# Optimization experiments

Hardware: AMD Instinct MI355X
Metric: run time of the kernel (lower is better)

## Reference

```python
import jax, jax.numpy as jnp
import numpy as np

B = 64        # graphs per batch
N_ATOMS = 16384   # atoms per graph
N_GLOBAL = 8      # global (virtual) nodes per graph
EPS = 1e-8


def setup_inputs() -> dict:
    key = jax.random.key(0)
    k1, k2, k3 = jax.random.split(key, 3)
    N = B * N_ATOMS
    G = B * N_GLOBAL
    atom_positions = jax.random.normal(k1, (N, 3), dtype=jnp.float32)
    pred_pos_global_node = jax.random.normal(k2, (G, 3), dtype=jnp.float32)
    true_direction_vectors = jax.random.normal(k3, (N, 3), dtype=jnp.float32)
    # uniform sorted batch assignment (equal-sized graphs)
    atom_batch_index = jnp.repeat(jnp.arange(B, dtype=jnp.int64), N_ATOMS)
    global_node_batch_index = jnp.repeat(jnp.arange(B, dtype=jnp.int64), N_GLOBAL)
    return {
        "atom_positions": atom_positions,
        "pred_pos_global_node": pred_pos_global_node,
        "true_direction_vectors": true_direction_vectors,
        "atom_batch_index": atom_batch_index,
        "global_node_batch_index": global_node_batch_index,
        "num_graphs": B,
    }


def reference(atom_positions, pred_pos_global_node, true_direction_vectors,
              atom_batch_index, global_node_batch_index, num_graphs):
    # Uniform batching: reshape ragged segments into dense [B, n] / [B, G].
    N = atom_positions.shape[0]
    Gt = pred_pos_global_node.shape[0]
    n = N // num_graphs
    G = Gt // num_graphs
    atoms = atom_positions.reshape(num_graphs, 1, n, 3)          # [B,1,n,3]
    tdir = true_direction_vectors.reshape(num_graphs, 1, n, 3)   # [B,1,n,3]
    gpos = pred_pos_global_node.reshape(num_graphs, G, 1, 3)     # [B,G,1,3]
    pdir = gpos - atoms                                           # [B,G,n,3] pred direction vectors
    num = jnp.sum(tdir * pdir, axis=-1)                           # [B,G,n]
    den = jnp.maximum(
        jnp.linalg.norm(tdir, axis=-1) * jnp.linalg.norm(pdir, axis=-1), EPS)
    cos = num / den                                               # [B,G,n]
    cosine_losses = 1.0 - jnp.mean(cos, axis=-1)                  # [B,G]
    min_idx = jnp.argmin(cosine_losses, axis=-1)                  # [B]
    min_loss = jnp.min(cosine_losses, axis=-1)                    # [B]
    return jnp.mean(min_loss), min_idx
```

## Files before the change

### kernel.cpp

```cpp
#include <hip/hip_runtime.h>

constexpr int B_GRAPHS = 64;
constexpr int N_PER_GRAPH = 16384;
constexpr int GPN = 8;
constexpr int THREADS = 256;
constexpr int ATOMS_PER_THREAD = 4;
constexpr int BLOCKS_PER_GRAPH = N_PER_GRAPH / (THREADS * ATOMS_PER_THREAD);
constexpr int NBLOCKS = B_GRAPHS * BLOCKS_PER_GRAPH;

__global__ __launch_bounds__(THREADS) void cos_partial(
    const float* __restrict__ atom_pos,
    const float* __restrict__ gpos,
    const float* __restrict__ tdir,
    float* __restrict__ partials)
{
    const int b  = blockIdx.x / BLOCKS_PER_GRAPH;
    const int tg = blockIdx.x * THREADS + threadIdx.x;

    const float4* ap4 = (const float4*)atom_pos;
    const float4* td4 = (const float4*)tdir;
    const size_t fb = (size_t)tg * 3;
    const float4 a0 = ap4[fb + 0], a1 = ap4[fb + 1], a2 = ap4[fb + 2];
    const float4 t0 = td4[fb + 0], t1 = td4[fb + 1], t2 = td4[fb + 2];

    float gx[GPN], gy[GPN], gz[GPN];
    const float* gp = gpos + (size_t)b * GPN * 3;
#pragma unroll
    for (int g = 0; g < GPN; ++g) {
        gx[g] = gp[g * 3 + 0];
        gy[g] = gp[g * 3 + 1];
        gz[g] = gp[g * 3 + 2];
    }

    const float ax[4] = {a0.x, a0.w, a1.z, a2.y};
    const float ay[4] = {a0.y, a1.x, a1.w, a2.z};
    const float az[4] = {a0.z, a1.y, a2.x, a2.w};
    const float tx[4] = {t0.x, t0.w, t1.z, t2.y};
    const float ty[4] = {t0.y, t1.x, t1.w, t2.z};
    const float tz[4] = {t0.z, t1.y, t2.x, t2.w};

    float accg[GPN];
#pragma unroll
    for (int g = 0; g < GPN; ++g) accg[g] = 0.0f;

#pragma unroll
    for (int a = 0; a < 4; ++a) {
        const float tn2 = fmaf(tx[a], tx[a], fmaf(ty[a], ty[a], tz[a] * tz[a]));
        const float itn = __builtin_amdgcn_rsqf(fmaxf(tn2, 1e-20f));
#pragma unroll
        for (int g = 0; g < GPN; ++g) {
            const float dx = gx[g] - ax[a];
            const float dy = gy[g] - ay[a];
            const float dz = gz[g] - az[a];
            const float dot = fmaf(tx[a], dx, fmaf(ty[a], dy, tz[a] * dz));
            const float pn2 = fmaf(dx, dx, fmaf(dy, dy, dz * dz));
            const float ipn = __builtin_amdgcn_rsqf(fmaxf(pn2, 1e-20f));
            accg[g] = fmaf(dot * itn, ipn, accg[g]);
        }
    }

    const int lane = threadIdx.x & 63;
    const int wave = threadIdx.x >> 6;
#pragma unroll
    for (int g = 0; g < GPN; ++g) {
        float v = accg[g];
#pragma unroll
        for (int off = 32; off > 0; off >>= 1)
            v += __shfl_xor(v, off);
        accg[g] = v;
    }

    __shared__ float lsum[THREADS / 64][GPN];
    if (lane == 0) {
#pragma unroll
        for (int g = 0; g < GPN; ++g) lsum[wave][g] = accg[g];
    }
    __syncthreads();
    if (threadIdx.x < GPN) {
        const int g = threadIdx.x;
        float s = 0.0f;
#pragma unroll
        for (int w = 0; w < THREADS / 64; ++w) s += lsum[w][g];
        partials[(size_t)blockIdx.x * GPN + g] = s;
    }
}

__global__ __launch_bounds__(512) void finalize(
    const float* __restrict__ partials,
    float* __restrict__ out)
{
    __shared__ float sums[B_GRAPHS * GPN];
    const int t = threadIdx.x;
    const int b = t >> 3, g = t & 7;
    float s = 0.0f;
#pragma unroll
    for (int c = 0; c < BLOCKS_PER_GRAPH; ++c)
        s += partials[((size_t)(b * BLOCKS_PER_GRAPH + c)) * GPN + g];
    sums[t] = s;
    __syncthreads();

    if (t < B_GRAPHS) {
        float minloss = 1e30f;
        int minidx = 0;
#pragma unroll
        for (int g2 = 0; g2 < GPN; ++g2) {
            const float loss = 1.0f - sums[t * GPN + g2] * (1.0f / (float)N_PER_GRAPH);
            if (loss < minloss) {
                minloss = loss;
                minidx = g2;
            }
        }
        out[1 + t] = (float)minidx;
        float v = minloss;
#pragma unroll
        for (int off = 32; off > 0; off >>= 1)
            v += __shfl_down(v, off);
        if (t == 0) out[0] = v * (1.0f / (float)B_GRAPHS);
    }
}

extern "C" void kernel_launch(void* const* d_in, const int* in_sizes, int n_in,
                              void* d_out, int out_size, void* d_ws, size_t ws_size,
                              hipStream_t stream) {
    const float* atom_pos = (const float*)d_in[0];
    const float* gpos     = (const float*)d_in[1];
    const float* tdir     = (const float*)d_in[2];

    float* partials = (float*)d_ws;

    cos_partial<<<NBLOCKS, THREADS, 0, stream>>>(atom_pos, gpos, tdir, partials);
    finalize<<<1, 512, 0, stream>>>(partials, (float*)d_out);
}
```

Before: 85.31 us.

## Fuse finalize into main kernel via last-block ticket and halve atoms per thread

New measurement: 150.6 us. 1.77x slower.

```diff
diff --git a/kernel.cpp b/kernel.cpp
--- a/kernel.cpp
+++ b/kernel.cpp
@@ -4,24 +4,27 @@
 constexpr int N_PER_GRAPH = 16384;
 constexpr int GPN = 8;
 constexpr int THREADS = 256;
-constexpr int ATOMS_PER_THREAD = 4;
+constexpr int ATOMS_PER_THREAD = 2;
 constexpr int BLOCKS_PER_GRAPH = N_PER_GRAPH / (THREADS * ATOMS_PER_THREAD);
 constexpr int NBLOCKS = B_GRAPHS * BLOCKS_PER_GRAPH;
+constexpr size_t PARTIALS_FLOATS = (size_t)NBLOCKS * GPN;
 
-__global__ __launch_bounds__(THREADS) void cos_partial(
+__global__ __launch_bounds__(THREADS) void cos_fused(
     const float* __restrict__ atom_pos,
     const float* __restrict__ gpos,
     const float* __restrict__ tdir,
-    float* __restrict__ partials)
+    float* __restrict__ partials,
+    unsigned int* __restrict__ ticket,
+    float* __restrict__ out)
 {
     const int b  = blockIdx.x / BLOCKS_PER_GRAPH;
     const int tg = blockIdx.x * THREADS + threadIdx.x;
 
-    const float4* ap4 = (const float4*)atom_pos;
-    const float4* td4 = (const float4*)tdir;
+    const float2* ap2 = (const float2*)atom_pos;
+    const float2* td2 = (const float2*)tdir;
     const size_t fb = (size_t)tg * 3;
-    const float4 a0 = ap4[fb + 0], a1 = ap4[fb + 1], a2 = ap4[fb + 2];
-    const float4 t0 = td4[fb + 0], t1 = td4[fb + 1], t2 = td4[fb + 2];
+    const float2 a0 = ap2[fb + 0], a1 = ap2[fb + 1], a2 = ap2[fb + 2];
+    const float2 t0 = td2[fb + 0], t1 = td2[fb + 1], t2 = td2[fb + 2];
 
     float gx[GPN], gy[GPN], gz[GPN];
     const float* gp = gpos + (size_t)b * GPN * 3;
@@ -32,19 +35,19 @@
         gz[g] = gp[g * 3 + 2];
     }
 
-    const float ax[4] = {a0.x, a0.w, a1.z, a2.y};
-    const float ay[4] = {a0.y, a1.x, a1.w, a2.z};
-    const float az[4] = {a0.z, a1.y, a2.x, a2.w};
-    const float tx[4] = {t0.x, t0.w, t1.z, t2.y};
-    const float ty[4] = {t0.y, t1.x, t1.w, t2.z};
-    const float tz[4] = {t0.z, t1.y, t2.x, t2.w};
+    const float ax[2] = {a0.x, a1.y};
+    const float ay[2] = {a0.y, a2.x};
+    const float az[2] = {a1.x, a2.y};
+    const float tx[2] = {t0.x, t1.y};
+    const float ty[2] = {t0.y, t2.x};
+    const float tz[2] = {t1.x, t2.y};
 
     float accg[GPN];
 #pragma unroll
     for (int g = 0; g < GPN; ++g) accg[g] = 0.0f;
 
 #pragma unroll
-    for (int a = 0; a < 4; ++a) {
+    for (int a = 0; a < 2; ++a) {
         const float tn2 = fmaf(tx[a], tx[a], fmaf(ty[a], ty[a], tz[a] * tz[a]));
         const float itn = __builtin_amdgcn_rsqf(fmaxf(tn2, 1e-20f));
 #pragma unroll
@@ -59,63 +62,78 @@
         }
     }
 
-    const int lane = threadIdx.x & 63;
-    const int wave = threadIdx.x >> 6;
 #pragma unroll
     for (int g = 0; g < GPN; ++g) {
         float v = accg[g];
-#pragma unroll
-        for (int off = 32; off > 0; off >>= 1)
-            v += __shfl_xor(v, off);
+        v += __shfl_xor(v, 8);
+        v += __shfl_xor(v, 16);
+        v += __shfl_xor(v, 32);
         accg[g] = v;
     }
+    const int lane = threadIdx.x & 63;
+    const int wave = threadIdx.x >> 6;
+    const int myg = lane >> 3;
+    float s = accg[0];
+#pragma unroll
+    for (int g = 1; g < GPN; ++g) s = (myg == g) ? accg[g] : s;
+    s += __shfl_xor(s, 1);
+    s += __shfl_xor(s, 2);
+    s += __shfl_xor(s, 4);
 
     __shared__ float lsum[THREADS / 64][GPN];
-    if (lane == 0) {
-#pragma unroll
-        for (int g = 0; g < GPN; ++g) lsum[wave][g] = accg[g];
+    __shared__ float sums[B_GRAPHS * GPN];
+    __shared__ unsigned int s_isLast;
+    if ((lane & 7) == 0) lsum[wave][myg] = s;
+    __syncthreads();
+
+    if (threadIdx.x < GPN) {
+        const int g = threadIdx.x;
+        const float bs = lsum[0][g] + lsum[1][g] + lsum[2][g] + lsum[3][g];
+        __hip_atomic_store(&partials[(size_t)blockIdx.x * GPN + g], bs,
+                           __ATOMIC_RELAXED, __HIP_MEMORY_SCOPE_AGENT);
     }
     __syncthreads();
-    if (threadIdx.x < GPN) {
-        const int g = threadIdx.x;
-        float s = 0.0f;
+
+    if (threadIdx.x == 0) {
+        __threadfence();
+        const unsigned int old = __hip_atomic_fetch_add(
+            ticket, 1u, __ATOMIC_ACQ_REL, __HIP_MEMORY_SCOPE_AGENT);
+        s_isLast = (old == (unsigned int)(NBLOCKS - 1)) ? 1u : 0u;
+    }
+    __syncthreads();
+    if (s_isLast == 0u) return;
+
+    __threadfence();
+    for (int p = threadIdx.x; p < B_GRAPHS * GPN; p += THREADS) {
+        const int bb = p >> 3, g = p & 7;
+        float s2 = 0.0f;
 #pragma unroll
-        for (int w = 0; w < THREADS / 64; ++w) s += lsum[w][g];
-        partials[(size_t)blockIdx.x * GPN + g] = s;
+        for (int c = 0; c < BLOCKS_PER_GRAPH; ++c)
+            s2 += __hip_atomic_load(
+                &partials[(size_t)(bb * BLOCKS_PER_GRAPH + c) * GPN + g],
+                __ATOMIC_RELAXED, __HIP_MEMORY_SCOPE_AGENT);
+        sums[p] = s2;
     }
-}
-
-__global__ __launch_bounds__(512) void finalize(
-    const float* __restrict__ partials,
-    float* __restrict__ out)
-{
-    __shared__ float sums[B_GRAPHS * GPN];
-    const int t = threadIdx.x;
-    const int b = t >> 3, g = t & 7;
-    float s = 0.0f;
-#pragma unroll
-    for (int c = 0; c < BLOCKS_PER_GRAPH; ++c)
-        s += partials[((size_t)(b * BLOCKS_PER_GRAPH + c)) * GPN + g];
-    sums[t] = s;
     __syncthreads();
 
-    if (t < B_GRAPHS) {
+    if (threadIdx.x < B_GRAPHS) {
+        const int bb = threadIdx.x;
         float minloss = 1e30f;
         int minidx = 0;
 #pragma unroll
-        for (int g2 = 0; g2 < GPN; ++g2) {
-            const float loss = 1.0f - sums[t * GPN + g2] * (1.0f / (float)N_PER_GRAPH);
+        for (int g = 0; g < GPN; ++g) {
+            const float loss = 1.0f - sums[bb * GPN + g] * (1.0f / (float)N_PER_GRAPH);
             if (loss < minloss) {
                 minloss = loss;
-                minidx = g2;
+                minidx = g;
             }
         }
-        out[1 + t] = (float)minidx;
+        out[1 + bb] = (float)minidx;
         float v = minloss;
 #pragma unroll
         for (int off = 32; off > 0; off >>= 1)
             v += __shfl_down(v, off);
-        if (t == 0) out[0] = v * (1.0f / (float)B_GRAPHS);
+        if (bb == 0) out[0] = v * (1.0f / (float)B_GRAPHS);
     }
 }
 
@@ -126,8 +144,10 @@
     const float* gpos     = (const float*)d_in[1];
     const float* tdir     = (const float*)d_in[2];
 
-    float* partials = (float*)d_ws;
+    float* partials      = (float*)d_ws;
+    unsigned int* ticket = (unsigned int*)((char*)d_ws + PARTIALS_FLOATS * sizeof(float));
 
-    cos_partial<<<NBLOCKS, THREADS, 0, stream>>>(atom_pos, gpos, tdir, partials);
-    finalize<<<1, 512, 0, stream>>>(partials, (float*)d_out);
+    hipMemsetAsync(ticket, 0, sizeof(unsigned int), stream);
+    cos_fused<<<NBLOCKS, THREADS, 0, stream>>>(
+        atom_pos, gpos, tdir, partials, ticket, (float*)d_out);
 }
```

## Halve atoms per thread and use transposed butterfly wave reduction

Applied to the files above, without the earlier changes.

Result: no change. 83.87 us (-1.7%).

```diff
diff --git a/kernel.cpp b/kernel.cpp
--- a/kernel.cpp
+++ b/kernel.cpp
@@ -4,7 +4,7 @@
 constexpr int N_PER_GRAPH = 16384;
 constexpr int GPN = 8;
 constexpr int THREADS = 256;
-constexpr int ATOMS_PER_THREAD = 4;
+constexpr int ATOMS_PER_THREAD = 2;
 constexpr int BLOCKS_PER_GRAPH = N_PER_GRAPH / (THREADS * ATOMS_PER_THREAD);
 constexpr int NBLOCKS = B_GRAPHS * BLOCKS_PER_GRAPH;
 
@@ -17,11 +17,11 @@
     const int b  = blockIdx.x / BLOCKS_PER_GRAPH;
     const int tg = blockIdx.x * THREADS + threadIdx.x;
 
-    const float4* ap4 = (const float4*)atom_pos;
-    const float4* td4 = (const float4*)tdir;
+    const float2* ap2 = (const float2*)atom_pos;
+    const float2* td2 = (const float2*)tdir;
     const size_t fb = (size_t)tg * 3;
-    const float4 a0 = ap4[fb + 0], a1 = ap4[fb + 1], a2 = ap4[fb + 2];
-    const float4 t0 = td4[fb + 0], t1 = td4[fb + 1], t2 = td4[fb + 2];
+    const float2 a0 = ap2[fb + 0], a1 = ap2[fb + 1], a2 = ap2[fb + 2];
+    const float2 t0 = td2[fb + 0], t1 = td2[fb + 1], t2 = td2[fb + 2];
 
     float gx[GPN], gy[GPN], gz[GPN];
     const float* gp = gpos + (size_t)b * GPN * 3;
@@ -32,19 +32,19 @@
         gz[g] = gp[g * 3 + 2];
     }
 
-    const float ax[4] = {a0.x, a0.w, a1.z, a2.y};
-    const float ay[4] = {a0.y, a1.x, a1.w, a2.z};
-    const float az[4] = {a0.z, a1.y, a2.x, a2.w};
-    const float tx[4] = {t0.x, t0.w, t1.z, t2.y};
-    const float ty[4] = {t0.y, t1.x, t1.w, t2.z};
-    const float tz[4] = {t0.z, t1.y, t2.x, t2.w};
+    const float ax[2] = {a0.x, a1.y};
+    const float ay[2] = {a0.y, a2.x};
+    const float az[2] = {a1.x, a2.y};
+    const float tx[2] = {t0.x, t1.y};
+    const float ty[2] = {t0.y, t2.x};
+    const float tz[2] = {t1.x, t2.y};
 
     float accg[GPN];
 #pragma unroll
     for (int g = 0; g < GPN; ++g) accg[g] = 0.0f;
 
 #pragma unroll
-    for (int a = 0; a < 4; ++a) {
+    for (int a = 0; a < 2; ++a) {
         const float tn2 = fmaf(tx[a], tx[a], fmaf(ty[a], ty[a], tz[a] * tz[a]));
         const float itn = __builtin_amdgcn_rsqf(fmaxf(tn2, 1e-20f));
 #pragma unroll
@@ -59,29 +59,31 @@
         }
     }
 
-    const int lane = threadIdx.x & 63;
-    const int wave = threadIdx.x >> 6;
 #pragma unroll
     for (int g = 0; g < GPN; ++g) {
         float v = accg[g];
-#pragma unroll
-        for (int off = 32; off > 0; off >>= 1)
-            v += __shfl_xor(v, off);
+        v += __shfl_xor(v, 8);
+        v += __shfl_xor(v, 16);
+        v += __shfl_xor(v, 32);
         accg[g] = v;
     }
+    const int lane = threadIdx.x & 63;
+    const int wave = threadIdx.x >> 6;
+    const int myg = lane >> 3;
+    float s = accg[0];
+#pragma unroll
+    for (int g = 1; g < GPN; ++g) s = (myg == g) ? accg[g] : s;
+    s += __shfl_xor(s, 1);
+    s += __shfl_xor(s, 2);
+    s += __shfl_xor(s, 4);
 
     __shared__ float lsum[THREADS / 64][GPN];
-    if (lane == 0) {
-#pragma unroll
-        for (int g = 0; g < GPN; ++g) lsum[wave][g] = accg[g];
-    }
+    if ((lane & 7) == 0) lsum[wave][myg] = s;
     __syncthreads();
     if (threadIdx.x < GPN) {
         const int g = threadIdx.x;
-        float s = 0.0f;
-#pragma unroll
-        for (int w = 0; w < THREADS / 64; ++w) s += lsum[w][g];
-        partials[(size_t)blockIdx.x * GPN + g] = s;
+        partials[(size_t)blockIdx.x * GPN + g] =
+            lsum[0][g] + lsum[1][g] + lsum[2][g] + lsum[3][g];
     }
 }
 
```
